# Performance work log

Hardware: AMD Instinct MI355X
Metric: run time of the kernel (lower is better)

The kernel has to match this reference:

```python
import jax, jax.numpy as jnp
import numpy as np


def setup_inputs() -> dict:
    key = jax.random.key(0)
    ks = jax.random.split(key, 6)
    b, l, d, n = 4, 2048, 1024, 16
    scale_d = 1.0 / np.sqrt(d)
    x = jax.random.normal(ks[0], (b, l, d), dtype=jnp.float32)
    W1 = jax.random.normal(ks[1], (d, d), dtype=jnp.float32) * scale_d
    b1 = jnp.zeros((d,), dtype=jnp.float32)
    W2 = jax.random.normal(ks[2], (n, d), dtype=jnp.float32) * scale_d
    b2 = jnp.zeros((n,), dtype=jnp.float32)
    W3 = jax.random.normal(ks[3], (n, d), dtype=jnp.float32) * scale_d
    b3 = jnp.zeros((n,), dtype=jnp.float32)
    A = jax.random.normal(ks[4], (d, n), dtype=jnp.float32) * np.sqrt(2.0 / (d + n))
    return {"x": x, "W1": W1, "b1": b1, "W2": W2, "b2": b2, "W3": W3, "b3": b3, "A": A}


def reference(x, W1, b1, W2, b2, W3, b3, A):
    # delta = softplus(fc1(x)); B = fc2(x); C = fc3(x)
    delta = jax.nn.softplus(jnp.einsum('bld,ed->ble', x, W1) + b1)   # (b,l,d)
    B = jnp.einsum('bld,nd->bln', x, W2) + b2                         # (b,l,n)
    C = jnp.einsum('bld,nd->bln', x, W3) + b3                         # (b,l,n)
    # Discretization: dB = delta \otimes B; dA = exp(delta \otimes A).
    # In the original forward, h is zero-initialized so dA * h == 0 exactly
    # (for both values and gradients); h_new = x[...,None] * dB.
    dB = jnp.einsum('bld,bln->bldn', delta, B)                        # (b,l,d,n)
    h = x[..., None] * dB                                             # (b,l,d,n)
    y = jnp.einsum('bln,bldn->bld', C, h)                             # (b,l,d)
    return y
```

## Files before the change

kernel.cpp:

```cpp
#include <hip/hip_runtime.h>
#include <hip/hip_bf16.h>

typedef __attribute__((ext_vector_type(8))) short bf16x8;
typedef __attribute__((ext_vector_type(8))) unsigned short u16x8;
typedef __attribute__((ext_vector_type(4))) unsigned short u16x4;
typedef __attribute__((ext_vector_type(4))) float f32x4;

#define DDIM 1024
#define BM 128
#define BN 128
#define BK 64

__device__ __forceinline__ void gload_lds16(const void* g, void* l) {
  __builtin_amdgcn_global_load_lds((const __attribute__((address_space(1))) void*)g,
                                   (__attribute__((address_space(3))) void*)l,
                                   16, 0, 0);
}

__device__ __forceinline__ unsigned short f2bf(float f) {
  unsigned int u = __float_as_uint(f);
  unsigned int r = (u + 0x7FFFu + ((u >> 16) & 1u)) >> 16;
  return (unsigned short)r;
}

__global__ __launch_bounds__(256) void s6_convert(
    const float* __restrict__ X, const float* __restrict__ W1,
    const float* __restrict__ W2, const float* __restrict__ W3,
    unsigned short* __restrict__ Xbf, unsigned short* __restrict__ W1bf,
    unsigned short* __restrict__ W2bf, unsigned short* __restrict__ W3bf)
{
  const int i   = blockIdx.x * 256 + threadIdx.x;
  const int row = i >> 8;
  const int off = (i & 255) * 4;

  const float* src;
  unsigned short* dst;
  if (row < 8192)      { src = X  + (size_t)row * DDIM;        dst = Xbf  + (size_t)row * DDIM; }
  else if (row < 9216) { int r = row - 8192; src = W1 + (size_t)r * DDIM; dst = W1bf + (size_t)r * DDIM; }
  else if (row < 9232) { int r = row - 9216; src = W2 + (size_t)r * DDIM; dst = W2bf + (size_t)r * DDIM; }
  else                 { int r = row - 9232; src = W3 + (size_t)r * DDIM; dst = W3bf + (size_t)r * DDIM; }

  const float4 v = *reinterpret_cast<const float4*>(src + off);
  u16x4 o;
  o[0] = f2bf(v.x); o[1] = f2bf(v.y); o[2] = f2bf(v.z); o[3] = f2bf(v.w);
  *reinterpret_cast<u16x4*>(dst + off) = o;
}

__global__ __launch_bounds__(512, 4) void s6_main_fused(
    const unsigned short* __restrict__ Xbf,
    const unsigned short* __restrict__ W1bf,
    const unsigned short* __restrict__ W2bf,
    const unsigned short* __restrict__ W3bf,
    const float* __restrict__ b1,
    const float* __restrict__ b2,
    const float* __restrict__ b3,
    float* __restrict__ Y)
{
  __shared__ __align__(16) unsigned short lds[2 * 8192 + 2 * 12288];
  unsigned short* AB = lds;
  unsigned short* BB = lds + 2 * 8192;

  const int tid  = threadIdx.x;
  const int wid  = tid >> 6;
  const int lane = tid & 63;
  const int tile = (blockIdx.x & 7) * 64 + (blockIdx.x >> 3);
  const int rb   = tile >> 3;
  const int cb   = tile & 7;
  const int row0 = rb * BM;
  const int col0 = cb * BN;
  const int wr = wid >> 1, wc = wid & 1;

  const f32x4 z4 = {0.f, 0.f, 0.f, 0.f};
  f32x4 acc[2][4];
  #pragma unroll
  for (int i = 0; i < 2; ++i)
    #pragma unroll
    for (int j = 0; j < 4; ++j)
      acc[i][j] = z4;
  f32x4 accS[2] = {z4, z4};

  const int srow = tid >> 3;
  const int sdch = (lane & 7) ^ (lane >> 3);
  const unsigned short* gaBase = Xbf  + (size_t)(row0 + srow) * DDIM + sdch * 8;
  const unsigned short* gbBase = W1bf + (size_t)(col0 + srow) * DDIM + sdch * 8;
  const int sub = srow;
  const unsigned short* gwsrc;
  if (sub < 16)      gwsrc = W2bf + (size_t)sub * DDIM;
  else if (sub < 32) gwsrc = W3bf + (size_t)(sub - 16) * DDIM;
  else               gwsrc = W2bf + (size_t)(sub & 15) * DDIM;
  const unsigned short* gwBase = gwsrc + sdch * 8;

  const int fr = lane & 15;
  const int swz0 = (((lane >> 4) + 0) ^ (fr & 7)) * 8;
  const int swz1 = (((lane >> 4) + 4) ^ (fr & 7)) * 8;

#define STAGE(BUF, KEL) do {                                                   \
    const unsigned short* sa_ = gaBase + (KEL);                                \
    const unsigned short* sb_ = gbBase + (KEL);                                \
    unsigned short* la_ = AB + (BUF) * 8192  + wid * 512;                      \
    unsigned short* lb_ = BB + (BUF) * 12288 + wid * 512;                      \
    gload_lds16(sa_,              la_);                                        \
    gload_lds16(sa_ + 64 * DDIM,  la_ + 4096);                                 \
    gload_lds16(sb_,              lb_);                                        \
    gload_lds16(sb_ + 64 * DDIM,  lb_ + 4096);                                 \
    gload_lds16(gwBase + (KEL),   lb_ + 8192);                                 \
  } while (0)

#define COMPUTE(PAR) do {                                                      \
    const unsigned short* Al = AB + (PAR) * 8192;                              \
    const unsigned short* Bl = BB + (PAR) * 12288;                             \
    _Pragma("unroll")                                                          \
    for (int ks = 0; ks < 2; ++ks) {                                           \
      const int swz = ks ? swz1 : swz0;                                        \
      bf16x8 a0 = *reinterpret_cast<const bf16x8*>(&Al[(wr*32 +  0 + fr)*BK + swz]); \
      bf16x8 a1 = *reinterpret_cast<const bf16x8*>(&Al[(wr*32 + 16 + fr)*BK + swz]); \
      bf16x8 g0 = *reinterpret_cast<const bf16x8*>(&Bl[(wc*64 +  0 + fr)*BK + swz]); \
      bf16x8 g1 = *reinterpret_cast<const bf16x8*>(&Bl[(wc*64 + 16 + fr)*BK + swz]); \
      bf16x8 g2 = *reinterpret_cast<const bf16x8*>(&Bl[(wc*64 + 32 + fr)*BK + swz]); \
      bf16x8 g3 = *reinterpret_cast<const bf16x8*>(&Bl[(wc*64 + 48 + fr)*BK + swz]); \
      bf16x8 wf = *reinterpret_cast<const bf16x8*>(&Bl[(128 + wc*16 + fr)*BK + swz]); \
      __builtin_amdgcn_s_setprio(1);                                           \
      acc[0][0] = __builtin_amdgcn_mfma_f32_16x16x32_bf16(a0, g0, acc[0][0], 0, 0, 0); \
      acc[0][1] = __builtin_amdgcn_mfma_f32_16x16x32_bf16(a0, g1, acc[0][1], 0, 0, 0); \
      acc[0][2] = __builtin_amdgcn_mfma_f32_16x16x32_bf16(a0, g2, acc[0][2], 0, 0, 0); \
      acc[0][3] = __builtin_amdgcn_mfma_f32_16x16x32_bf16(a0, g3, acc[0][3], 0, 0, 0); \
      acc[1][0] = __builtin_amdgcn_mfma_f32_16x16x32_bf16(a1, g0, acc[1][0], 0, 0, 0); \
      acc[1][1] = __builtin_amdgcn_mfma_f32_16x16x32_bf16(a1, g1, acc[1][1], 0, 0, 0); \
      acc[1][2] = __builtin_amdgcn_mfma_f32_16x16x32_bf16(a1, g2, acc[1][2], 0, 0, 0); \
      acc[1][3] = __builtin_amdgcn_mfma_f32_16x16x32_bf16(a1, g3, acc[1][3], 0, 0, 0); \
      accS[0]   = __builtin_amdgcn_mfma_f32_16x16x32_bf16(a0, wf, accS[0], 0, 0, 0); \
      accS[1]   = __builtin_amdgcn_mfma_f32_16x16x32_bf16(a1, wf, accS[1], 0, 0, 0); \
      __builtin_amdgcn_s_setprio(0);                                           \
    }                                                                          \
  } while (0)

#define STEP(J, PAR) do {                                                      \
    if ((J) < 15) {                                                            \
      STAGE((PAR) ^ 1, ((J) + 1) * BK);                                        \
      asm volatile("s_waitcnt vmcnt(5)" ::: "memory");                         \
    } else {                                                                   \
      asm volatile("s_waitcnt vmcnt(0)" ::: "memory");                         \
    }                                                                          \
    __builtin_amdgcn_s_barrier();                                              \
    __builtin_amdgcn_sched_barrier(0);                                         \
    COMPUTE(PAR);                                                              \
    __builtin_amdgcn_s_barrier();                                              \
  } while (0)

  STAGE(0, 0);
  asm volatile("s_waitcnt vmcnt(0)" ::: "memory");
  __builtin_amdgcn_s_barrier();

  for (int jj = 0; jj < 16; jj += 2) {
    STEP(jj, 0);
    STEP(jj + 1, 1);
  }
#undef STEP
#undef COMPUTE
#undef STAGE

  float* sEx = (float*)lds;
  const int n_  = lane & 15;
  const int rgp = (lane >> 4) * 4;
  const float bSelf = (wc == 0 ? b2[n_] : b3[n_]);
  #pragma unroll
  for (int m = 0; m < 2; ++m)
    #pragma unroll
    for (int q = 0; q < 4; ++q)
      sEx[(wc * 128 + wr * 32 + m * 16 + rgp + q) * 17 + n_] = accS[m][q] + bSelf;
  __syncthreads();

  float sv[2][4];
  #pragma unroll
  for (int m = 0; m < 2; ++m) {
    #pragma unroll
    for (int q = 0; q < 4; ++q) {
      const float other = sEx[((wc ^ 1) * 128 + wr * 32 + m * 16 + rgp + q) * 17 + n_];
      float p = (accS[m][q] + bSelf) * other;
      p += __shfl_xor(p, 1, 64);
      p += __shfl_xor(p, 2, 64);
      p += __shfl_xor(p, 4, 64);
      p += __shfl_xor(p, 8, 64);
      sv[m][q] = p;
    }
  }

  #pragma unroll
  for (int m = 0; m < 2; ++m) {
    #pragma unroll
    for (int q = 0; q < 4; ++q) {
      const int gr = row0 + wr * 32 + m * 16 + rgp + q;
      const float svv = sv[m][q];
      const size_t rbase = (size_t)gr * DDIM;
      #pragma unroll
      for (int n = 0; n < 4; ++n) {
        const int gc = col0 + wc * 64 + n * 16 + fr;
        const float z  = acc[m][n][q] + b1[gc];
        const float e  = exp2f(-1.44269504f * fabsf(z));
        const float sp = fmaxf(z, 0.f) + 0.69314718f * log2f(1.f + e);
        const float xv = __bfloat162float(*(const __hip_bfloat16*)&Xbf[rbase + gc]);
        Y[rbase + gc] = xv * svv * sp;
      }
    }
  }
}

extern "C" void kernel_launch(void* const* d_in, const int* in_sizes, int n_in,
                              void* d_out, int out_size, void* d_ws, size_t ws_size,
                              hipStream_t stream) {
  const float* x  = (const float*)d_in[0];
  const float* W1 = (const float*)d_in[1];
  const float* b1 = (const float*)d_in[2];
  const float* W2 = (const float*)d_in[3];
  const float* b2 = (const float*)d_in[4];
  const float* W3 = (const float*)d_in[5];
  const float* b3 = (const float*)d_in[6];

  char* ws = (char*)d_ws;
  unsigned short* Xbf  = (unsigned short*)(ws);
  unsigned short* W1bf = (unsigned short*)(ws + 16777216);
  unsigned short* W2bf = (unsigned short*)(ws + 16777216 + 2097152);
  unsigned short* W3bf = (unsigned short*)(ws + 16777216 + 2097152 + 32768);

  s6_convert<<<9248, 256, 0, stream>>>(x, W1, W2, W3, Xbf, W1bf, W2bf, W3bf);
  s6_main_fused<<<512, 512, 0, stream>>>(Xbf, W1bf, W2bf, W3bf, b1, b2, b3,
                                         (float*)d_out);
}
```

Before: 43.61 us.

## Fuse X fp32-to-bf16 conversion into GEMM A-tile loading via registers

```diff
diff --git a/kernel.cpp b/kernel.cpp
--- a/kernel.cpp
+++ b/kernel.cpp
@@ -2,7 +2,6 @@
 #include <hip/hip_bf16.h>
 
 typedef __attribute__((ext_vector_type(8))) short bf16x8;
-typedef __attribute__((ext_vector_type(8))) unsigned short u16x8;
 typedef __attribute__((ext_vector_type(4))) unsigned short u16x4;
 typedef __attribute__((ext_vector_type(4))) float f32x4;
 
@@ -23,11 +22,11 @@
   return (unsigned short)r;
 }
 
-__global__ __launch_bounds__(256) void s6_convert(
-    const float* __restrict__ X, const float* __restrict__ W1,
-    const float* __restrict__ W2, const float* __restrict__ W3,
-    unsigned short* __restrict__ Xbf, unsigned short* __restrict__ W1bf,
-    unsigned short* __restrict__ W2bf, unsigned short* __restrict__ W3bf)
+__global__ __launch_bounds__(256) void s6_convert_w(
+    const float* __restrict__ W1, const float* __restrict__ W2,
+    const float* __restrict__ W3,
+    unsigned short* __restrict__ W1bf, unsigned short* __restrict__ W2bf,
+    unsigned short* __restrict__ W3bf)
 {
   const int i   = blockIdx.x * 256 + threadIdx.x;
   const int row = i >> 8;
@@ -35,10 +34,9 @@
 
   const float* src;
   unsigned short* dst;
-  if (row < 8192)      { src = X  + (size_t)row * DDIM;        dst = Xbf  + (size_t)row * DDIM; }
-  else if (row < 9216) { int r = row - 8192; src = W1 + (size_t)r * DDIM; dst = W1bf + (size_t)r * DDIM; }
-  else if (row < 9232) { int r = row - 9216; src = W2 + (size_t)r * DDIM; dst = W2bf + (size_t)r * DDIM; }
-  else                 { int r = row - 9232; src = W3 + (size_t)r * DDIM; dst = W3bf + (size_t)r * DDIM; }
+  if (row < 1024)      { src = W1 + (size_t)row * DDIM;          dst = W1bf + (size_t)row * DDIM; }
+  else if (row < 1040) { int r = row - 1024; src = W2 + (size_t)r * DDIM; dst = W2bf + (size_t)r * DDIM; }
+  else                 { int r = row - 1040; src = W3 + (size_t)r * DDIM; dst = W3bf + (size_t)r * DDIM; }
 
   const float4 v = *reinterpret_cast<const float4*>(src + off);
   u16x4 o;
@@ -47,7 +45,7 @@
 }
 
 __global__ __launch_bounds__(512, 4) void s6_main_fused(
-    const unsigned short* __restrict__ Xbf,
+    const float* __restrict__ X,
     const unsigned short* __restrict__ W1bf,
     const unsigned short* __restrict__ W2bf,
     const unsigned short* __restrict__ W3bf,
@@ -79,28 +77,48 @@
       acc[i][j] = z4;
   f32x4 accS[2] = {z4, z4};
 
+  const int arow  = tid >> 4;
+  const int acol  = (tid & 15) * 4;
+  const int ac8   = (tid & 15) >> 1;
+  const int ahalf = (tid & 1) * 4;
+  const float* gA = X + (size_t)(row0 + arow) * DDIM + acol;
+
   const int srow = tid >> 3;
   const int sdch = (lane & 7) ^ (lane >> 3);
-  const unsigned short* gaBase = Xbf  + (size_t)(row0 + srow) * DDIM + sdch * 8;
   const unsigned short* gbBase = W1bf + (size_t)(col0 + srow) * DDIM + sdch * 8;
-  const int sub = srow;
   const unsigned short* gwsrc;
-  if (sub < 16)      gwsrc = W2bf + (size_t)sub * DDIM;
-  else if (sub < 32) gwsrc = W3bf + (size_t)(sub - 16) * DDIM;
-  else               gwsrc = W2bf + (size_t)(sub & 15) * DDIM;
+  if (srow < 16)      gwsrc = W2bf + (size_t)srow * DDIM;
+  else if (srow < 32) gwsrc = W3bf + (size_t)(srow - 16) * DDIM;
+  else                gwsrc = W2bf + (size_t)(srow & 15) * DDIM;
   const unsigned short* gwBase = gwsrc + sdch * 8;
 
   const int fr = lane & 15;
   const int swz0 = (((lane >> 4) + 0) ^ (fr & 7)) * 8;
   const int swz1 = (((lane >> 4) + 4) ^ (fr & 7)) * 8;
 
-#define STAGE(BUF, KEL) do {                                                   \
-    const unsigned short* sa_ = gaBase + (KEL);                                \
+  float4 av[4];
+
+#define ALOAD(KEL) do {                                                        \
+    _Pragma("unroll")                                                          \
+    for (int j = 0; j < 4; ++j)                                                \
+      av[j] = *reinterpret_cast<const float4*>(gA + (size_t)(j * 32) * DDIM + (KEL)); \
+  } while (0)
+
+#define AWRITE(BUF) do {                                                       \
+    _Pragma("unroll")                                                          \
+    for (int j = 0; j < 4; ++j) {                                              \
+      const int row_ = arow + j * 32;                                          \
+      const int off_ = row_ * 64 + ((ac8 ^ (row_ & 7)) << 3) + ahalf;          \
+      uint2 w_;                                                                \
+      asm("v_cvt_pk_bf16_f32 %0, %1, %2" : "=v"(w_.x) : "v"(av[j].x), "v"(av[j].y)); \
+      asm("v_cvt_pk_bf16_f32 %0, %1, %2" : "=v"(w_.y) : "v"(av[j].z), "v"(av[j].w)); \
+      *reinterpret_cast<uint2*>(AB + (BUF) * 8192 + off_) = w_;                \
+    }                                                                          \
+  } while (0)
+
+#define SBW(BUF, KEL) do {                                                     \
     const unsigned short* sb_ = gbBase + (KEL);                                \
-    unsigned short* la_ = AB + (BUF) * 8192  + wid * 512;                      \
     unsigned short* lb_ = BB + (BUF) * 12288 + wid * 512;                      \
-    gload_lds16(sa_,              la_);                                        \
-    gload_lds16(sa_ + 64 * DDIM,  la_ + 4096);                                 \
     gload_lds16(sb_,              lb_);                                        \
     gload_lds16(sb_ + 64 * DDIM,  lb_ + 4096);                                 \
     gload_lds16(gwBase + (KEL),   lb_ + 8192);                                 \
@@ -134,30 +152,32 @@
     }                                                                          \
   } while (0)
 
-#define STEP(J, PAR) do {                                                      \
-    if ((J) < 15) {                                                            \
-      STAGE((PAR) ^ 1, ((J) + 1) * BK);                                        \
-      asm volatile("s_waitcnt vmcnt(5)" ::: "memory");                         \
-    } else {                                                                   \
-      asm volatile("s_waitcnt vmcnt(0)" ::: "memory");                         \
-    }                                                                          \
-    __builtin_amdgcn_s_barrier();                                              \
-    __builtin_amdgcn_sched_barrier(0);                                         \
-    COMPUTE(PAR);                                                              \
-    __builtin_amdgcn_s_barrier();                                              \
-  } while (0)
-
-  STAGE(0, 0);
-  asm volatile("s_waitcnt vmcnt(0)" ::: "memory");
-  __builtin_amdgcn_s_barrier();
-
-  for (int jj = 0; jj < 16; jj += 2) {
-    STEP(jj, 0);
-    STEP(jj + 1, 1);
+  ALOAD(0);
+  SBW(0, 0);
+  asm volatile("s_waitcnt vmcnt(3)" ::: "memory");
+  AWRITE(0);
+  __syncthreads();
+
+  for (int t = 0; t < 16; ++t) {
+    const int cur = t & 1;
+    const int nb  = cur ^ 1;
+    const int kn  = (t + 1) * BK;
+    if (t < 15) {
+      ALOAD(kn);
+      SBW(nb, kn);
+    }
+    __builtin_amdgcn_sched_barrier(0);
+    COMPUTE(cur);
+    if (t < 15) {
+      asm volatile("s_waitcnt vmcnt(3)" ::: "memory");
+      AWRITE(nb);
+    }
+    __syncthreads();
   }
-#undef STEP
+#undef ALOAD
+#undef AWRITE
+#undef SBW
 #undef COMPUTE
-#undef STAGE
 
   float* sEx = (float*)lds;
   const int n_  = lane & 15;
@@ -198,7 +218,7 @@
         const float z  = acc[m][n][q] + b1[gc];
         const float e  = exp2f(-1.44269504f * fabsf(z));
         const float sp = fmaxf(z, 0.f) + 0.69314718f * log2f(1.f + e);
-        const float xv = __bfloat162float(*(const __hip_bfloat16*)&Xbf[rbase + gc]);
+        const float xv = X[rbase + gc];
         Y[rbase + gc] = xv * svv * sp;
       }
     }
@@ -217,12 +237,11 @@
   const float* b3 = (const float*)d_in[6];
 
   char* ws = (char*)d_ws;
-  unsigned short* Xbf  = (unsigned short*)(ws);
-  unsigned short* W1bf = (unsigned short*)(ws + 16777216);
-  unsigned short* W2bf = (unsigned short*)(ws + 16777216 + 2097152);
-  unsigned short* W3bf = (unsigned short*)(ws + 16777216 + 2097152 + 32768);
-
-  s6_convert<<<9248, 256, 0, stream>>>(x, W1, W2, W3, Xbf, W1bf, W2bf, W3bf);
-  s6_main_fused<<<512, 512, 0, stream>>>(Xbf, W1bf, W2bf, W3bf, b1, b2, b3,
+  unsigned short* W1bf = (unsigned short*)(ws);
+  unsigned short* W2bf = (unsigned short*)(ws + 2097152);
+  unsigned short* W3bf = (unsigned short*)(ws + 2097152 + 32768);
+
+  s6_convert_w<<<1056, 256, 0, stream>>>(W1, W2, W3, W1bf, W2bf, W3bf);
+  s6_main_fused<<<512, 512, 0, stream>>>(x, W1bf, W2bf, W3bf, b1, b2, b3,
                                          (float*)d_out);
 }
```

After: 43.21 us (median of 2 runs). No clear change (-0.9%).

## Load X fragments directly into registers and halve workgroup to four waves

Applied to the files above, without the earlier changes.

```diff
diff --git a/kernel.cpp b/kernel.cpp
--- a/kernel.cpp
+++ b/kernel.cpp
@@ -2,7 +2,6 @@
 #include <hip/hip_bf16.h>
 
 typedef __attribute__((ext_vector_type(8))) short bf16x8;
-typedef __attribute__((ext_vector_type(8))) unsigned short u16x8;
 typedef __attribute__((ext_vector_type(4))) unsigned short u16x4;
 typedef __attribute__((ext_vector_type(4))) float f32x4;
 
@@ -46,7 +45,7 @@
   *reinterpret_cast<u16x4*>(dst + off) = o;
 }
 
-__global__ __launch_bounds__(512, 4) void s6_main_fused(
+__global__ __launch_bounds__(256, 3) void s6_main_fused(
     const unsigned short* __restrict__ Xbf,
     const unsigned short* __restrict__ W1bf,
     const unsigned short* __restrict__ W2bf,
@@ -56,9 +55,8 @@
     const float* __restrict__ b3,
     float* __restrict__ Y)
 {
-  __shared__ __align__(16) unsigned short lds[2 * 8192 + 2 * 12288];
-  unsigned short* AB = lds;
-  unsigned short* BB = lds + 2 * 8192;
+  __shared__ __align__(16) unsigned short BB[2 * 10240];
+  float* sEx = (float*)BB;
 
   const int tid  = threadIdx.x;
   const int wid  = tid >> 6;
@@ -71,111 +69,109 @@
   const int wr = wid >> 1, wc = wid & 1;
 
   const f32x4 z4 = {0.f, 0.f, 0.f, 0.f};
-  f32x4 acc[2][4];
-  #pragma unroll
-  for (int i = 0; i < 2; ++i)
+  f32x4 acc[4][4];
+  #pragma unroll
+  for (int i = 0; i < 4; ++i)
     #pragma unroll
     for (int j = 0; j < 4; ++j)
       acc[i][j] = z4;
-  f32x4 accS[2] = {z4, z4};
+  f32x4 accS[4] = {z4, z4, z4, z4};
+
+  bf16x8 ar[2][4];
 
   const int srow = tid >> 3;
-  const int sdch = (lane & 7) ^ (lane >> 3);
-  const unsigned short* gaBase = Xbf  + (size_t)(row0 + srow) * DDIM + sdch * 8;
+  const int sdch = (tid & 7) ^ (srow & 7);
   const unsigned short* gbBase = W1bf + (size_t)(col0 + srow) * DDIM + sdch * 8;
-  const int sub = srow;
-  const unsigned short* gwsrc;
-  if (sub < 16)      gwsrc = W2bf + (size_t)sub * DDIM;
-  else if (sub < 32) gwsrc = W3bf + (size_t)(sub - 16) * DDIM;
-  else               gwsrc = W2bf + (size_t)(sub & 15) * DDIM;
-  const unsigned short* gwBase = gwsrc + sdch * 8;
+  const unsigned short* gwBase =
+      (srow < 16 ? W2bf + (size_t)srow * DDIM : W3bf + (size_t)(srow - 16) * DDIM) + sdch * 8;
 
   const int fr = lane & 15;
+  const unsigned short* gAF = Xbf + (size_t)(row0 + wr * 64 + fr) * DDIM + (lane >> 4) * 8;
+
   const int swz0 = (((lane >> 4) + 0) ^ (fr & 7)) * 8;
   const int swz1 = (((lane >> 4) + 4) ^ (fr & 7)) * 8;
 
-#define STAGE(BUF, KEL) do {                                                   \
-    const unsigned short* sa_ = gaBase + (KEL);                                \
-    const unsigned short* sb_ = gbBase + (KEL);                                \
-    unsigned short* la_ = AB + (BUF) * 8192  + wid * 512;                      \
-    unsigned short* lb_ = BB + (BUF) * 12288 + wid * 512;                      \
-    gload_lds16(sa_,              la_);                                        \
-    gload_lds16(sa_ + 64 * DDIM,  la_ + 4096);                                 \
-    gload_lds16(sb_,              lb_);                                        \
-    gload_lds16(sb_ + 64 * DDIM,  lb_ + 4096);                                 \
-    gload_lds16(gwBase + (KEL),   lb_ + 8192);                                 \
+#define SBW(BUF, KEL) do {                                                     \
+    unsigned short* lb_ = BB + (BUF) * 10240 + wid * 512;                      \
+    gload_lds16(gbBase + (KEL),                lb_);                           \
+    gload_lds16(gbBase + (KEL) + 32 * DDIM,    lb_ + 2048);                    \
+    gload_lds16(gbBase + (KEL) + 64 * DDIM,    lb_ + 4096);                    \
+    gload_lds16(gbBase + (KEL) + 96 * DDIM,    lb_ + 6144);                    \
+    gload_lds16(gwBase + (KEL),                lb_ + 8192);                    \
   } while (0)
 
+#define ALOAD(KEL) do {                                                        \
+    _Pragma("unroll")                                                          \
+    for (int ks = 0; ks < 2; ++ks)                                             \
+      _Pragma("unroll")                                                        \
+      for (int m = 0; m < 4; ++m)                                              \
+        ar[ks][m] = *reinterpret_cast<const bf16x8*>(                          \
+            gAF + (size_t)(m * 16) * DDIM + ks * 32 + (KEL));                  \
+  } while (0)
+
 #define COMPUTE(PAR) do {                                                      \
-    const unsigned short* Al = AB + (PAR) * 8192;                              \
-    const unsigned short* Bl = BB + (PAR) * 12288;                             \
+    const unsigned short* Bl = BB + (PAR) * 10240;                             \
     _Pragma("unroll")                                                          \
     for (int ks = 0; ks < 2; ++ks) {                                           \
       const int swz = ks ? swz1 : swz0;                                        \
-      bf16x8 a0 = *reinterpret_cast<const bf16x8*>(&Al[(wr*32 +  0 + fr)*BK + swz]); \
-      bf16x8 a1 = *reinterpret_cast<const bf16x8*>(&Al[(wr*32 + 16 + fr)*BK + swz]); \
       bf16x8 g0 = *reinterpret_cast<const bf16x8*>(&Bl[(wc*64 +  0 + fr)*BK + swz]); \
       bf16x8 g1 = *reinterpret_cast<const bf16x8*>(&Bl[(wc*64 + 16 + fr)*BK + swz]); \
       bf16x8 g2 = *reinterpret_cast<const bf16x8*>(&Bl[(wc*64 + 32 + fr)*BK + swz]); \
       bf16x8 g3 = *reinterpret_cast<const bf16x8*>(&Bl[(wc*64 + 48 + fr)*BK + swz]); \
       bf16x8 wf = *reinterpret_cast<const bf16x8*>(&Bl[(128 + wc*16 + fr)*BK + swz]); \
       __builtin_amdgcn_s_setprio(1);                                           \
-      acc[0][0] = __builtin_amdgcn_mfma_f32_16x16x32_bf16(a0, g0, acc[0][0], 0, 0, 0); \
-      acc[0][1] = __builtin_amdgcn_mfma_f32_16x16x32_bf16(a0, g1, acc[0][1], 0, 0, 0); \
-      acc[0][2] = __builtin_amdgcn_mfma_f32_16x16x32_bf16(a0, g2, acc[0][2], 0, 0, 0); \
-      acc[0][3] = __builtin_amdgcn_mfma_f32_16x16x32_bf16(a0, g3, acc[0][3], 0, 0, 0); \
-      acc[1][0] = __builtin_amdgcn_mfma_f32_16x16x32_bf16(a1, g0, acc[1][0], 0, 0, 0); \
-      acc[1][1] = __builtin_amdgcn_mfma_f32_16x16x32_bf16(a1, g1, acc[1][1], 0, 0, 0); \
-      acc[1][2] = __builtin_amdgcn_mfma_f32_16x16x32_bf16(a1, g2, acc[1][2], 0, 0, 0); \
-      acc[1][3] = __builtin_amdgcn_mfma_f32_16x16x32_bf16(a1, g3, acc[1][3], 0, 0, 0); \
-      accS[0]   = __builtin_amdgcn_mfma_f32_16x16x32_bf16(a0, wf, accS[0], 0, 0, 0); \
-      accS[1]   = __builtin_amdgcn_mfma_f32_16x16x32_bf16(a1, wf, accS[1], 0, 0, 0); \
+      _Pragma("unroll")                                                        \
+      for (int m = 0; m < 4; ++m) {                                            \
+        acc[m][0] = __builtin_amdgcn_mfma_f32_16x16x32_bf16(ar[ks][m], g0, acc[m][0], 0, 0, 0); \
+        acc[m][1] = __builtin_amdgcn_mfma_f32_16x16x32_bf16(ar[ks][m], g1, acc[m][1], 0, 0, 0); \
+        acc[m][2] = __builtin_amdgcn_mfma_f32_16x16x32_bf16(ar[ks][m], g2, acc[m][2], 0, 0, 0); \
+        acc[m][3] = __builtin_amdgcn_mfma_f32_16x16x32_bf16(ar[ks][m], g3, acc[m][3], 0, 0, 0); \
+        accS[m]   = __builtin_amdgcn_mfma_f32_16x16x32_bf16(ar[ks][m], wf, accS[m], 0, 0, 0); \
+      }                                                                        \
       __builtin_amdgcn_s_setprio(0);                                           \
     }                                                                          \
   } while (0)
 
-#define STEP(J, PAR) do {                                                      \
-    if ((J) < 15) {                                                            \
-      STAGE((PAR) ^ 1, ((J) + 1) * BK);                                        \
-      asm volatile("s_waitcnt vmcnt(5)" ::: "memory");                         \
-    } else {                                                                   \
-      asm volatile("s_waitcnt vmcnt(0)" ::: "memory");                         \
-    }                                                                          \
-    __builtin_amdgcn_s_barrier();                                              \
-    __builtin_amdgcn_sched_barrier(0);                                         \
-    COMPUTE(PAR);                                                              \
-    __builtin_amdgcn_s_barrier();                                              \
-  } while (0)
-
-  STAGE(0, 0);
-  asm volatile("s_waitcnt vmcnt(0)" ::: "memory");
+  SBW(0, 0);
+  ALOAD(0);
+  asm volatile("s_waitcnt vmcnt(8)" ::: "memory");
   __builtin_amdgcn_s_barrier();
-
-  for (int jj = 0; jj < 16; jj += 2) {
-    STEP(jj, 0);
-    STEP(jj + 1, 1);
+  __builtin_amdgcn_sched_barrier(0);
+
+  for (int t = 0; t < 16; ++t) {
+    const int cur = t & 1;
+    const int kn  = (t + 1) * BK;
+    if (t < 15) SBW(cur ^ 1, kn);
+    COMPUTE(cur);
+    if (t < 15) {
+      ALOAD(kn);
+      asm volatile("s_waitcnt vmcnt(8)" ::: "memory");
+    }
+    __builtin_amdgcn_s_barrier();
+    __builtin_amdgcn_sched_barrier(0);
   }
-#undef STEP
+#undef SBW
+#undef ALOAD
 #undef COMPUTE
-#undef STAGE
-
-  float* sEx = (float*)lds;
+
+  __syncthreads();
+
   const int n_  = lane & 15;
   const int rgp = (lane >> 4) * 4;
   const float bSelf = (wc == 0 ? b2[n_] : b3[n_]);
   #pragma unroll
-  for (int m = 0; m < 2; ++m)
+  for (int m = 0; m < 4; ++m)
     #pragma unroll
     for (int q = 0; q < 4; ++q)
-      sEx[(wc * 128 + wr * 32 + m * 16 + rgp + q) * 17 + n_] = accS[m][q] + bSelf;
+      sEx[(wc * 128 + wr * 64 + m * 16 + rgp + q) * 17 + n_] = accS[m][q] + bSelf;
   __syncthreads();
 
-  float sv[2][4];
-  #pragma unroll
-  for (int m = 0; m < 2; ++m) {
+  float sv[4][4];
+  #pragma unroll
+  for (int m = 0; m < 4; ++m) {
     #pragma unroll
     for (int q = 0; q < 4; ++q) {
-      const float other = sEx[((wc ^ 1) * 128 + wr * 32 + m * 16 + rgp + q) * 17 + n_];
+      const float other = sEx[((wc ^ 1) * 128 + wr * 64 + m * 16 + rgp + q) * 17 + n_];
       float p = (accS[m][q] + bSelf) * other;
       p += __shfl_xor(p, 1, 64);
       p += __shfl_xor(p, 2, 64);
@@ -186,10 +182,10 @@
   }
 
   #pragma unroll
-  for (int m = 0; m < 2; ++m) {
+  for (int m = 0; m < 4; ++m) {
     #pragma unroll
     for (int q = 0; q < 4; ++q) {
-      const int gr = row0 + wr * 32 + m * 16 + rgp + q;
+      const int gr = row0 + wr * 64 + m * 16 + rgp + q;
       const float svv = sv[m][q];
       const size_t rbase = (size_t)gr * DDIM;
       #pragma unroll
@@ -223,6 +219,6 @@
   unsigned short* W3bf = (unsigned short*)(ws + 16777216 + 2097152 + 32768);
 
   s6_convert<<<9248, 256, 0, stream>>>(x, W1, W2, W3, Xbf, W1bf, W2bf, W3bf);
-  s6_main_fused<<<512, 512, 0, stream>>>(Xbf, W1bf, W2bf, W3bf, b1, b2, b3,
+  s6_main_fused<<<512, 256, 0, stream>>>(Xbf, W1bf, W2bf, W3bf, b1, b2, b3,
                                          (float*)d_out);
 }
```

Result: slower. 61.81 us (+41.7%).
